# Optimization experiments

Measured on AMD Instinct MI355X. Metric: run time of the kernel, lower is better.

## Reference

```python
import jax, jax.numpy as jnp
import numpy as np
from jax import lax

B, C, H, W = 8, 128, 128, 128


def setup_inputs() -> dict:
    key = jax.random.key(0)
    ks = jax.random.split(key, 10)
    s = 0.02
    return {
        "x": jax.random.normal(ks[0], (B, C, H, W), jnp.float32),
        "ln_w": jnp.ones((C,), jnp.float32),
        "ln_b": jnp.zeros((C,), jnp.float32),
        "qkv_w": jax.random.normal(ks[1], (3 * C, C, 1, 1), jnp.float32) * s,
        "qkv_b": jnp.zeros((3 * C,), jnp.float32),
        "dw_w": jax.random.normal(ks[2], (3 * C, 1, 3, 3), jnp.float32) * s,
        "dw_b": jnp.zeros((3 * C,), jnp.float32),
        "proj_w": jax.random.normal(ks[3], (C, C, 1, 1), jnp.float32) * s,
        "proj_b": jnp.zeros((C,), jnp.float32),
        "temp1": jnp.ones((1, 1), jnp.float32),
        "temp2": jnp.ones((1, 1), jnp.float32),
    }


def reference(x, ln_w, ln_b, qkv_w, qkv_b, dw_w, dw_b, proj_w, proj_b, temp1, temp2):
    Cd = x.shape[1]

    def ln(t):  # WithBias LayerNorm over channel dim (unbiased=False var)
        mu = t.mean(axis=1, keepdims=True)
        var = ((t - mu) ** 2).mean(axis=1, keepdims=True)
        return (t - mu) / jnp.sqrt(var + 1e-5) * ln_w[None, :, None, None] + ln_b[None, :, None, None]

    def conv1(t, w, b):  # 1x1 conv
        return jnp.einsum('bchw,oc->bohw', t, w[:, :, 0, 0]) + b[None, :, None, None]

    def dwc(t):  # depthwise 3x3, pad 1
        y = lax.conv_general_dilated(t, dw_w, (1, 1), ((1, 1), (1, 1)),
                                     dimension_numbers=('NCHW', 'OIHW', 'NCHW'),
                                     feature_group_count=t.shape[1])
        return y + dw_b[None, :, None, None]

    def l2n(t):  # F.normalize over last axis, eps=1e-12
        return t / jnp.maximum(jnp.linalg.norm(t, axis=-1, keepdims=True), 1e-12)

    # ---- stage 1: pool over H, attention over W (channel-pooled) ----
    qkv = dwc(conv1(ln(x), qkv_w, qkv_b))
    q1, k1, v1 = qkv[:, :Cd], qkv[:, Cd:2 * Cd], qkv[:, 2 * Cd:]
    q1 = l2n(q1.mean(axis=2)[:, None])           # [B,1,C,W]
    k1 = l2n(k1.max(axis=2)[:, None])            # [B,1,C,W]
    attn1 = jax.nn.softmax(jnp.einsum('bocw,bocv->bowv', q1, k1) * temp1, axis=-1)  # [B,1,W,W]
    out1 = jnp.einsum('bchw,bowv->bchv', v1, attn1)
    out1 = x + conv1(out1, proj_w, proj_b)

    # ---- stage 2: pool over C, attention over H ----
    qkv = dwc(conv1(ln(out1), qkv_w, qkv_b))
    q2, k2, v2 = qkv[:, :Cd], qkv[:, Cd:2 * Cd], qkv[:, 2 * Cd:]
    q2 = l2n(q2.mean(axis=1)[:, None])           # [B,1,H,W]
    k2 = l2n(k2.mean(axis=1)[:, None])           # [B,1,H,W]
    attn2 = jax.nn.softmax(jnp.einsum('bohw,bogw->bohg', q2, k2) * temp2, axis=-1)  # [B,1,H,H]
    out2 = jnp.einsum('bchw,bohg->bcgw', v2, attn2)  # = (v^T @ attn)^T
    out = conv1(out2, proj_w, proj_b) + out1
    return out
```

## Files before the change

### kernel.cpp

```cpp
#include <hip/hip_runtime.h>

typedef __attribute__((ext_vector_type(8))) short bf16x8;
typedef __attribute__((ext_vector_type(4))) float f32x4;
typedef __attribute__((ext_vector_type(4))) unsigned short us4;
typedef __attribute__((ext_vector_type(4))) unsigned int u32x4;

static constexpr int CC = 128, NN = 16384;
static constexpr int O3 = 384;
static constexpr long long CN  = (long long)CC * NN;
static constexpr long long O3N = (long long)O3 * NN;

__device__ __forceinline__ float wave_sum(float v) {
  for (int o = 32; o; o >>= 1) v += __shfl_xor(v, o);
  return v;
}
__device__ __forceinline__ float wave_max(float v) {
  for (int o = 32; o; o >>= 1) v = fmaxf(v, __shfl_xor(v, o));
  return v;
}
__device__ __forceinline__ unsigned short f2bf(float f) {
  unsigned u = __float_as_uint(f);
  u += 0x7FFF + ((u >> 16) & 1);
  return (unsigned short)(u >> 16);
}
__device__ __forceinline__ float bf2f(unsigned short h) {
  return __uint_as_float((unsigned)h << 16);
}

__global__ __launch_bounds__(64) void k_prep(const float* __restrict__ qkvw,
                                             const float* __restrict__ qkvb,
                                             const float* __restrict__ lnw,
                                             const float* __restrict__ lnb,
                                             const float* __restrict__ projw,
                                             unsigned short* __restrict__ Aq,
                                             unsigned short* __restrict__ Ap,
                                             float* __restrict__ Svec,
                                             float* __restrict__ bias2) {
  int o = blockIdx.x, t = threadIdx.x;
  if (o < O3) {
    float w0 = qkvw[o * 128 + t], w1 = qkvw[o * 128 + t + 64];
    unsigned short h0 = f2bf(w0 * lnw[t]), h1 = f2bf(w1 * lnw[t + 64]);
    Aq[o * 128 + t] = h0; Aq[o * 128 + t + 64] = h1;
    float s = wave_sum(bf2f(h0) + bf2f(h1));
    float bs = wave_sum(w0 * lnb[t] + w1 * lnb[t + 64]);
    if (t == 0) { Svec[o] = s; bias2[o] = qkvb[o] + bs; }
  } else {
    int r = o - O3;
    Ap[r * 128 + t] = f2bf(projw[r * 128 + t]);
    Ap[r * 128 + t + 64] = f2bf(projw[r * 128 + t + 64]);
  }
}

__global__ __launch_bounds__(256) void k_stats(const float* __restrict__ in,
                                               float* __restrict__ mu,
                                               float* __restrict__ rs) {
  int p = blockIdx.x * 256 + threadIdx.x;
  int b = p >> 14, n = p & (NN - 1);
  const float* base = in + (size_t)b * CN + n;
  float s1 = 0.f, s2 = 0.f;
#pragma unroll 8
  for (int c = 0; c < CC; ++c) { float v = base[(size_t)c * NN]; s1 += v; s2 += v * v; }
  float m = s1 * (1.f / CC);
  float var = s2 * (1.f / CC) - m * m;
  mu[p] = m;
  rs[p] = rsqrtf(var + 1e-5f);
}

__global__ __launch_bounds__(256) void k_qkv_mfma(
    const float* __restrict__ x, const float* __restrict__ mu, const float* __restrict__ rs,
    const unsigned short* __restrict__ Aq, const float* __restrict__ Svec,
    const float* __restrict__ bias2, unsigned short* __restrict__ out, int b0) {
  __shared__ unsigned short Bs[64 * 128];
  int bz = blockIdx.z, bg = b0 + bz;
  int n0 = blockIdx.x * 64;
  int t = threadIdx.x, w = t >> 6, l = t & 63;
  int lr = l & 15, lg = l >> 4;
  const float* xb = x + (size_t)bg * CN + n0;

  {
    int n = t & 63, cb = t >> 6;
#pragma unroll
    for (int g = 0; g < 4; ++g) {
      int c8 = (cb * 4 + g) * 8;
      unsigned pk[4];
#pragma unroll
      for (int q = 0; q < 4; ++q) {
        unsigned short a = f2bf(xb[(size_t)(c8 + 2 * q) * NN + n]);
        unsigned short b = f2bf(xb[(size_t)(c8 + 2 * q + 1) * NN + n]);
        pk[q] = (unsigned)a | ((unsigned)b << 16);
      }
      int c8s = c8 ^ ((n & 7) << 3);
      *(u32x4*)&Bs[n * 128 + c8s] = *(const u32x4*)pk;
    }
  }
  __syncthreads();

  f32x4 acc[6][4];
#pragma unroll
  for (int i = 0; i < 6; ++i)
#pragma unroll
    for (int j = 0; j < 4; ++j) acc[i][j] = (f32x4){0.f, 0.f, 0.f, 0.f};

  const unsigned short* Abase = Aq + (size_t)(96 * w + lr) * 128 + lg * 8;
#pragma unroll
  for (int ks = 0; ks < 4; ++ks) {
    bf16x8 bfr[4];
#pragma unroll
    for (int j = 0; j < 4; ++j) {
      int row = 16 * j + lr;
      int col = (ks * 32 + lg * 8) ^ ((lr & 7) << 3);
      bfr[j] = *(const bf16x8*)&Bs[row * 128 + col];
    }
#pragma unroll
    for (int i = 0; i < 6; ++i) {
      bf16x8 afr = *(const bf16x8*)&Abase[(size_t)(16 * i) * 128 + ks * 32];
#pragma unroll
      for (int j = 0; j < 4; ++j)
        acc[i][j] = __builtin_amdgcn_mfma_f32_16x16x32_bf16(afr, bfr[j], acc[i][j], 0, 0, 0);
    }
  }

  float rsv[4], muv[4];
#pragma unroll
  for (int j = 0; j < 4; ++j) {
    int n = n0 + 16 * j + lr;
    rsv[j] = rs[(size_t)bg * NN + n];
    muv[j] = mu[(size_t)bg * NN + n];
  }
#pragma unroll
  for (int i = 0; i < 6; ++i) {
    int ob = 96 * w + 16 * i + lg * 4;
    float sv[4], bv[4];
#pragma unroll
    for (int r2 = 0; r2 < 4; ++r2) { sv[r2] = Svec[ob + r2]; bv[r2] = bias2[ob + r2]; }
#pragma unroll
    for (int j = 0; j < 4; ++j) {
      int n = n0 + 16 * j + lr;
      unsigned short* op = out + (size_t)bz * O3N + n;
#pragma unroll
      for (int r2 = 0; r2 < 4; ++r2)
        op[(size_t)(ob + r2) * NN] = f2bf(rsv[j] * (acc[i][j][r2] - muv[j] * sv[r2]) + bv[r2]);
    }
  }
}

__global__ __launch_bounds__(1024) void k_dwc(unsigned short* __restrict__ buf,
                                              const float* __restrict__ dww,
                                              const float* __restrict__ dwb,
                                              float* __restrict__ qm,
                                              float* __restrict__ km,
                                              int b0, int stage) {
  __shared__ unsigned short pl[130 * 144];
  __shared__ float red[32 * 128];
  int o = blockIdx.x, bz = blockIdx.y, bg = b0 + bz;
  int t = threadIdx.x;
  unsigned short* base = buf + (size_t)bz * O3N + (size_t)o * NN;
  unsigned* pl32 = (unsigned*)pl;

  for (int i = t; i < 1168; i += 1024) {
    int idx;
    if (i < 72) idx = i;
    else if (i < 144) idx = 129 * 72 + (i - 72);
    else { int j = i - 144; int row = (j >> 3) + 1; int s = j & 7;
           idx = row * 72 + (s < 4 ? s : 64 + s); }
    pl32[idx] = 0u;
  }
  __syncthreads();
#pragma unroll
  for (int r = 0; r < 2; ++r) {
    int idx = r * 1024 + t;
    int row = idx >> 4, c8 = (idx & 15) * 8;
    *(u32x4*)&pl[(row + 1) * 144 + 8 + c8] = *(const u32x4*)&base[row * 128 + c8];
  }
  __syncthreads();

  const float* wg = dww + o * 9;
  float w00 = wg[0], w01 = wg[1], w02 = wg[2];
  float w10 = wg[3], w11 = wg[4], w12 = wg[5];
  float w20 = wg[6], w21 = wg[7], w22 = wg[8];
  float bias = dwb[o];
  int mode = (stage == 0) ? (o < 128 ? 1 : (o < 256 ? 2 : 0)) : 0;
  int hh0 = t >> 5, w0 = (t & 31) * 4;
  float csum[4] = {0.f, 0.f, 0.f, 0.f};
  float cmax[4] = {-1e30f, -1e30f, -1e30f, -1e30f};

#pragma unroll
  for (int g = 0; g < 4; ++g) {
    int h = g * 32 + hh0;
    float a0 = bias, a1 = bias, a2 = bias, a3 = bias;
#pragma unroll
    for (int dr = 0; dr < 3; ++dr) {
      const unsigned short* rp = &pl[(h + dr) * 144];
      us4 cA = *(const us4*)&rp[w0 + 4];
      us4 cB = *(const us4*)&rp[w0 + 8];
      us4 cC = *(const us4*)&rp[w0 + 12];
      float f0 = bf2f(cA[3]), f1 = bf2f(cB[0]), f2 = bf2f(cB[1]);
      float f3 = bf2f(cB[2]), f4 = bf2f(cB[3]), f5 = bf2f(cC[0]);
      float wr0 = (dr == 0) ? w00 : (dr == 1 ? w10 : w20);
      float wr1 = (dr == 0) ? w01 : (dr == 1 ? w11 : w21);
      float wr2 = (dr == 0) ? w02 : (dr == 1 ? w12 : w22);
      a0 += f0 * wr0 + f1 * wr1 + f2 * wr2;
      a1 += f1 * wr0 + f2 * wr1 + f3 * wr2;
      a2 += f2 * wr0 + f3 * wr1 + f4 * wr2;
      a3 += f3 * wr0 + f4 * wr1 + f5 * wr2;
    }
    if (mode == 0) {
      us4 ov;
      ov[0] = f2bf(a0); ov[1] = f2bf(a1); ov[2] = f2bf(a2); ov[3] = f2bf(a3);
      *(us4*)&base[g * 4096 + t * 4] = ov;
    } else if (mode == 1) {
      csum[0] += a0; csum[1] += a1; csum[2] += a2; csum[3] += a3;
    } else {
      cmax[0] = fmaxf(cmax[0], a0); cmax[1] = fmaxf(cmax[1], a1);
      cmax[2] = fmaxf(cmax[2], a2); cmax[3] = fmaxf(cmax[3], a3);
    }
  }

  if (mode) {
    int j = t >> 5;
#pragma unroll
    for (int dx = 0; dx < 4; ++dx)
      red[j * 128 + w0 + dx] = (mode == 1) ? csum[dx] : cmax[dx];
    __syncthreads();
    if (t < 128) {
      float v = red[t];
      if (mode == 1) {
        for (int jj = 1; jj < 32; ++jj) v += red[jj * 128 + t];
        qm[(size_t)bg * NN + o * 128 + t] = v * (1.f / 128.f);
      } else {
        for (int jj = 1; jj < 32; ++jj) v = fmaxf(v, red[jj * 128 + t]);
        km[(size_t)bg * NN + (o - 128) * 128 + t] = v;
      }
    }
  }
}

__global__ __launch_bounds__(256) void k_reduce2(const unsigned short* __restrict__ qkv,
                                                 float* __restrict__ qm, float* __restrict__ km,
                                                 int b0) {
  int bz = blockIdx.y;
  int n = blockIdx.x * 256 + threadIdx.x;
  const unsigned short* base = qkv + (size_t)bz * O3N + n;
  float sq = 0.f, sk = 0.f;
#pragma unroll 4
  for (int c = 0; c < 128; ++c) {
    sq += bf2f(base[(size_t)c * NN]);
    sk += bf2f(base[(size_t)(c + 128) * NN]);
  }
  size_t off = (size_t)(b0 + bz) * NN + n;
  qm[off] = sq * (1.f / 128.f);
  km[off] = sk * (1.f / 128.f);
}

__global__ void k_norm2(float* __restrict__ qm, float* __restrict__ km, int row0) {
  float* buf = blockIdx.y ? km : qm;
  int r = row0 + blockIdx.x, t = threadIdx.x;
  float* p = buf + (size_t)r * 128;
  float v0 = p[t], v1 = p[t + 64];
  float s = wave_sum(v0 * v0 + v1 * v1);
  float sc = 1.f / fmaxf(sqrtf(s), 1e-12f);
  p[t] = v0 * sc;
  p[t + 64] = v1 * sc;
}

__global__ void k_attn1(const float* __restrict__ qm, const float* __restrict__ km,
                        const float* __restrict__ temp, unsigned short* __restrict__ attnT,
                        int b0) {
  int bg = b0 + blockIdx.y;
  int i = blockIdx.x, t = threadIdx.x;
  const float* qb = qm + (size_t)bg * NN;
  const float* kb = km + (size_t)bg * NN;
  __shared__ float qcol[128];
  __shared__ float wred[2];
  qcol[t] = qb[t * 128 + i];
  __syncthreads();
  float s = 0.f;
#pragma unroll 4
  for (int k = 0; k < 128; ++k) s += qcol[k] * kb[k * 128 + t];
  s *= temp[0];
  int wid = t >> 6, lane = t & 63;
  float mx = wave_max(s);
  if (lane == 0) wred[wid] = mx;
  __syncthreads();
  mx = fmaxf(wred[0], wred[1]);
  float pv = __expf(s - mx);
  __syncthreads();
  float sm = wave_sum(pv);
  if (lane == 0) wred[wid] = sm;
  __syncthreads();
  float denom = wred[0] + wred[1];
  attnT[(size_t)bg * NN + (size_t)t * 128 + i] = f2bf(pv / denom);
}

__global__ void k_attn2(const float* __restrict__ qm, const float* __restrict__ km,
                        const float* __restrict__ temp, unsigned short* __restrict__ attnT,
                        int b0) {
  int bg = b0 + blockIdx.y;
  int i = blockIdx.x, t = threadIdx.x;
  const float* qb = qm + (size_t)bg * NN + i * 128;
  const float* kb = km + (size_t)bg * NN + (size_t)t * 128;
  __shared__ float qrow[128];
  __shared__ float wred[2];
  qrow[t] = qb[t];
  __syncthreads();
  float s = 0.f;
#pragma unroll 4
  for (int w = 0; w < 128; ++w) s += qrow[w] * kb[w];
  s *= temp[0];
  int wid = t >> 6, lane = t & 63;
  float mx = wave_max(s);
  if (lane == 0) wred[wid] = mx;
  __syncthreads();
  mx = fmaxf(wred[0], wred[1]);
  float pv = __expf(s - mx);
  __syncthreads();
  float sm = wave_sum(pv);
  if (lane == 0) wred[wid] = sm;
  __syncthreads();
  float denom = wred[0] + wred[1];
  attnT[(size_t)bg * NN + (size_t)t * 128 + i] = f2bf(pv / denom);
}

__global__ __launch_bounds__(256) void k_apply1_mfma(unsigned short* __restrict__ buf,
                                                     const unsigned short* __restrict__ attnT,
                                                     int b0) {
  __shared__ unsigned short Al[128 * 136];
  __shared__ unsigned short Bl[128 * 136];
  int bz = blockIdx.z, bg = b0 + bz;
  int m0 = blockIdx.x * 128;
  int t = threadIdx.x, w = t >> 6, l = t & 63, lr = l & 15, lg = l >> 4;
  const unsigned short* asrc = buf + (size_t)bz * O3N + (size_t)256 * NN + (size_t)m0 * 128;
  const unsigned short* bsrc = attnT + (size_t)bg * NN;
#pragma unroll
  for (int r = 0; r < 8; ++r) {
    int idx = r * 256 + t;
    int row = idx >> 4, c8 = (idx & 15) * 8;
    *(u32x4*)&Al[row * 136 + c8] = *(const u32x4*)&asrc[row * 128 + c8];
    *(u32x4*)&Bl[row * 136 + c8] = *(const u32x4*)&bsrc[row * 128 + c8];
  }
  __syncthreads();
  f32x4 acc[2][8];
#pragma unroll
  for (int i = 0; i < 2; ++i)
#pragma unroll
    for (int j = 0; j < 8; ++j) acc[i][j] = (f32x4){0.f, 0.f, 0.f, 0.f};
#pragma unroll
  for (int ks = 0; ks < 4; ++ks) {
    bf16x8 bfr[8];
#pragma unroll
    for (int j = 0; j < 8; ++j)
      bfr[j] = *(const bf16x8*)&Bl[(16 * j + lr) * 136 + ks * 32 + lg * 8];
#pragma unroll
    for (int i = 0; i < 2; ++i) {
      bf16x8 afr = *(const bf16x8*)&Al[(32 * w + 16 * i + lr) * 136 + ks * 32 + lg * 8];
#pragma unroll
      for (int j = 0; j < 8; ++j)
        acc[i][j] = __builtin_amdgcn_mfma_f32_16x16x32_bf16(afr, bfr[j], acc[i][j], 0, 0, 0);
    }
  }
  unsigned short* ob = buf + (size_t)bz * O3N;
#pragma unroll
  for (int i = 0; i < 2; ++i)
#pragma unroll
    for (int j = 0; j < 8; ++j)
#pragma unroll
      for (int r2 = 0; r2 < 4; ++r2) {
        int m = m0 + 32 * w + 16 * i + lg * 4 + r2;
        int n = 16 * j + lr;
        ob[(size_t)m * 128 + n] = f2bf(acc[i][j][r2]);
      }
}

__global__ __launch_bounds__(256) void k_apply2_mfma(unsigned short* __restrict__ buf,
                                                     const unsigned short* __restrict__ attnT,
                                                     int b0) {
  __shared__ unsigned short At[128 * 136];
  __shared__ unsigned short Bt[128 * 136];
  int bz = blockIdx.z, bg = b0 + bz, c = blockIdx.x;
  int t = threadIdx.x, w = t >> 6, l = t & 63, lr = l & 15, lg = l >> 4;
  const unsigned short* vsrc = buf + (size_t)bz * O3N + (size_t)(256 + c) * NN;
  const unsigned short* asrc = attnT + (size_t)bg * NN;
#pragma unroll
  for (int r = 0; r < 8; ++r) {
    int idx = r * 256 + t;
    int row = idx >> 4, c8 = (idx & 15) * 8;
    *(u32x4*)&At[row * 136 + c8] = *(const u32x4*)&asrc[row * 128 + c8];
    us4 lo = *(const us4*)&vsrc[row * 128 + c8];
    us4 hi = *(const us4*)&vsrc[row * 128 + c8 + 4];
#pragma unroll
    for (int q = 0; q < 4; ++q) {
      Bt[(c8 + q) * 136 + row] = lo[q];
      Bt[(c8 + 4 + q) * 136 + row] = hi[q];
    }
  }
  __syncthreads();
  f32x4 acc[2][8];
#pragma unroll
  for (int i = 0; i < 2; ++i)
#pragma unroll
    for (int j = 0; j < 8; ++j) acc[i][j] = (f32x4){0.f, 0.f, 0.f, 0.f};
#pragma unroll
  for (int ks = 0; ks < 4; ++ks) {
    bf16x8 bfr[8];
#pragma unroll
    for (int j = 0; j < 8; ++j)
      bfr[j] = *(const bf16x8*)&Bt[(16 * j + lr) * 136 + ks * 32 + lg * 8];
#pragma unroll
    for (int i = 0; i < 2; ++i) {
      bf16x8 afr = *(const bf16x8*)&At[(32 * w + 16 * i + lr) * 136 + ks * 32 + lg * 8];
#pragma unroll
      for (int j = 0; j < 8; ++j)
        acc[i][j] = __builtin_amdgcn_mfma_f32_16x16x32_bf16(afr, bfr[j], acc[i][j], 0, 0, 0);
    }
  }
  unsigned short* ob = buf + (size_t)bz * O3N + (size_t)c * NN;
#pragma unroll
  for (int i = 0; i < 2; ++i)
#pragma unroll
    for (int j = 0; j < 8; ++j)
#pragma unroll
      for (int r2 = 0; r2 < 4; ++r2) {
        int g = 32 * w + 16 * i + lg * 4 + r2;
        int n = 16 * j + lr;
        ob[(size_t)g * 128 + n] = f2bf(acc[i][j][r2]);
      }
}

__global__ __launch_bounds__(256) void k_proj_mfma(
    const unsigned short* __restrict__ tin, const unsigned short* __restrict__ Ap,
    const float* __restrict__ pb, const float* __restrict__ res,
    float* __restrict__ dst, float* __restrict__ mu, float* __restrict__ rs,
    int b0, int do_stats) {
  __shared__ unsigned short Bs2[64 * 128];
  __shared__ float red1[64 * 17];
  __shared__ float red2[64 * 17];
  int bz = blockIdx.z, bg = b0 + bz;
  int n0 = blockIdx.x * 64;
  int t = threadIdx.x, w = t >> 6, l = t & 63, lr = l & 15, lg = l >> 4;
  const unsigned short* tb = tin + (size_t)bz * O3N + n0;

  {
    int n = t & 63, cb = t >> 6;
#pragma unroll
    for (int g = 0; g < 4; ++g) {
      int c8 = (cb * 4 + g) * 8;
      unsigned pk[4];
#pragma unroll
      for (int q = 0; q < 4; ++q) {
        unsigned short a = tb[(size_t)(c8 + 2 * q) * NN + n];
        unsigned short b = tb[(size_t)(c8 + 2 * q + 1) * NN + n];
        pk[q] = (unsigned)a | ((unsigned)b << 16);
      }
      int c8s = c8 ^ ((n & 7) << 3);
      *(u32x4*)&Bs2[n * 128 + c8s] = *(const u32x4*)pk;
    }
  }
  __syncthreads();

  f32x4 acc[2][4];
#pragma unroll
  for (int i = 0; i < 2; ++i)
#pragma unroll
    for (int j = 0; j < 4; ++j) acc[i][j] = (f32x4){0.f, 0.f, 0.f, 0.f};

  const unsigned short* Abase = Ap + (size_t)(32 * w + lr) * 128 + lg * 8;
#pragma unroll
  for (int ks = 0; ks < 4; ++ks) {
    bf16x8 bfr[4];
#pragma unroll
    for (int j = 0; j < 4; ++j) {
      int row = 16 * j + lr;
      int col = (ks * 32 + lg * 8) ^ ((lr & 7) << 3);
      bfr[j] = *(const bf16x8*)&Bs2[row * 128 + col];
    }
#pragma unroll
    for (int i = 0; i < 2; ++i) {
      bf16x8 afr = *(const bf16x8*)&Abase[(size_t)(16 * i) * 128 + ks * 32];
#pragma unroll
      for (int j = 0; j < 4; ++j)
        acc[i][j] = __builtin_amdgcn_mfma_f32_16x16x32_bf16(afr, bfr[j], acc[i][j], 0, 0, 0);
    }
  }

  float s1p[4] = {0.f, 0.f, 0.f, 0.f}, s2p[4] = {0.f, 0.f, 0.f, 0.f};
#pragma unroll
  for (int i = 0; i < 2; ++i) {
    int ob = 32 * w + 16 * i + lg * 4;
    float bv[4];
#pragma unroll
    for (int r2 = 0; r2 < 4; ++r2) bv[r2] = pb[ob + r2];
#pragma unroll
    for (int j = 0; j < 4; ++j) {
      int n = n0 + 16 * j + lr;
#pragma unroll
      for (int r2 = 0; r2 < 4; ++r2) {
        size_t off = (size_t)bg * CN + (size_t)(ob + r2) * NN + n;
        float val = acc[i][j][r2] + bv[r2] + res[off];
        dst[off] = val;
        s1p[j] += val;
        s2p[j] += val * val;
      }
    }
  }
  if (do_stats) {
#pragma unroll
    for (int j = 0; j < 4; ++j) {
      red1[(16 * j + lr) * 17 + (w * 4 + lg)] = s1p[j];
      red2[(16 * j + lr) * 17 + (w * 4 + lg)] = s2p[j];
    }
    __syncthreads();
    if (t < 64) {
      float s1 = 0.f, s2 = 0.f;
#pragma unroll
      for (int kk = 0; kk < 16; ++kk) { s1 += red1[t * 17 + kk]; s2 += red2[t * 17 + kk]; }
      float m = s1 * (1.f / 128.f);
      float var = s2 * (1.f / 128.f) - m * m;
      mu[(size_t)bg * NN + n0 + t] = m;
      rs[(size_t)bg * NN + n0 + t] = rsqrtf(var + 1e-5f);
    }
  }
}

extern "C" void kernel_launch(void* const* d_in, const int* in_sizes, int n_in,
                              void* d_out, int out_size, void* d_ws, size_t ws_size,
                              hipStream_t stream) {
  (void)in_sizes; (void)n_in; (void)out_size;
  const float* x     = (const float*)d_in[0];
  const float* lnw   = (const float*)d_in[1];
  const float* lnb   = (const float*)d_in[2];
  const float* qkvw  = (const float*)d_in[3];
  const float* qkvb  = (const float*)d_in[4];
  const float* dww   = (const float*)d_in[5];
  const float* dwb   = (const float*)d_in[6];
  const float* projw = (const float*)d_in[7];
  const float* projb = (const float*)d_in[8];
  const float* temp1 = (const float*)d_in[9];
  const float* temp2 = (const float*)d_in[10];
  float* out = (float*)d_out;
  float* ws = (float*)d_ws;

  auto needBytes = [&](int nb) {
    return ((size_t)nb * (O3N / 2) + 4ull * 131072 + 65536 + 768 + 24576 + 8192) * 4;
  };
  int NB = 8;
  while (NB > 1 && ws_size < needBytes(NB)) NB >>= 1;
  if (ws_size < needBytes(1)) return;

  unsigned short* convbuf = (unsigned short*)ws;
  float* mu = ws + (size_t)NB * (O3N / 2);
  float* rs = mu + 131072;
  float* qm = rs + 131072;
  float* km = qm + 131072;
  unsigned short* attnT = (unsigned short*)(km + 131072);
  float* Svec  = (float*)(attnT + 8ull * NN);
  float* bias2 = Svec + 384;
  unsigned short* Aq = (unsigned short*)(bias2 + 384);
  unsigned short* Ap = Aq + 49152;

  k_prep<<<512, 64, 0, stream>>>(qkvw, qkvb, lnw, lnb, projw, Aq, Ap, Svec, bias2);
  k_stats<<<512, 256, 0, stream>>>(x, mu, rs);

  for (int stage = 0; stage < 2; ++stage) {
    const float* src = stage ? out : x;
    for (int b0 = 0; b0 < 8; b0 += NB) {
      k_qkv_mfma<<<dim3(256, 1, NB), 256, 0, stream>>>(src, mu, rs, Aq, Svec, bias2, convbuf, b0);
      k_dwc<<<dim3(384, NB), 1024, 0, stream>>>(convbuf, dww, dwb, qm, km, b0, stage);
      if (stage == 1)
        k_reduce2<<<dim3(64, NB), 256, 0, stream>>>(convbuf, qm, km, b0);
      k_norm2<<<dim3(NB * 128, 2), 64, 0, stream>>>(qm, km, b0 * 128);
      if (stage == 0)
        k_attn1<<<dim3(128, NB), 128, 0, stream>>>(qm, km, temp1, attnT, b0);
      else
        k_attn2<<<dim3(128, NB), 128, 0, stream>>>(qm, km, temp2, attnT, b0);
      if (stage == 0)
        k_apply1_mfma<<<dim3(128, 1, NB), 256, 0, stream>>>(convbuf, attnT, b0);
      else
        k_apply2_mfma<<<dim3(128, 1, NB), 256, 0, stream>>>(convbuf, attnT, b0);
      const float* resp = stage ? out : x;
      k_proj_mfma<<<dim3(256, 1, NB), 256, 0, stream>>>(convbuf, Ap, projb, resp, out,
                                                        mu, rs, b0, stage == 0 ? 1 : 0);
    }
  }
}
```

Before: 338.8 us.

## Fuse stage-1 LayerNorm stats into QKV kernel and preload weight fragments

```diff
diff --git a/kernel.cpp b/kernel.cpp
--- a/kernel.cpp
+++ b/kernel.cpp
@@ -51,42 +51,44 @@
   }
 }
 
-__global__ __launch_bounds__(256) void k_stats(const float* __restrict__ in,
-                                               float* __restrict__ mu,
-                                               float* __restrict__ rs) {
-  int p = blockIdx.x * 256 + threadIdx.x;
-  int b = p >> 14, n = p & (NN - 1);
-  const float* base = in + (size_t)b * CN + n;
-  float s1 = 0.f, s2 = 0.f;
-#pragma unroll 8
-  for (int c = 0; c < CC; ++c) { float v = base[(size_t)c * NN]; s1 += v; s2 += v * v; }
-  float m = s1 * (1.f / CC);
-  float var = s2 * (1.f / CC) - m * m;
-  mu[p] = m;
-  rs[p] = rsqrtf(var + 1e-5f);
-}
-
-__global__ __launch_bounds__(256) void k_qkv_mfma(
+__global__ __launch_bounds__(256, 2) void k_qkv_mfma(
     const float* __restrict__ x, const float* __restrict__ mu, const float* __restrict__ rs,
     const unsigned short* __restrict__ Aq, const float* __restrict__ Svec,
-    const float* __restrict__ bias2, unsigned short* __restrict__ out, int b0) {
+    const float* __restrict__ bias2, unsigned short* __restrict__ out, int b0, int useg) {
   __shared__ unsigned short Bs[64 * 128];
+  __shared__ float muL[64], rsL[64];
   int bz = blockIdx.z, bg = b0 + bz;
   int n0 = blockIdx.x * 64;
   int t = threadIdx.x, w = t >> 6, l = t & 63;
   int lr = l & 15, lg = l >> 4;
   const float* xb = x + (size_t)bg * CN + n0;
 
+  bf16x8 afr[6][4];
+  {
+    const unsigned short* Abase = Aq + (size_t)(96 * w + lr) * 128 + lg * 8;
+#pragma unroll
+    for (int i = 0; i < 6; ++i)
+#pragma unroll
+      for (int ks = 0; ks < 4; ++ks)
+        afr[i][ks] = *(const bf16x8*)&Abase[(size_t)(16 * i) * 128 + ks * 32];
+  }
+
   {
     int n = t & 63, cb = t >> 6;
+    float xr[32];
+#pragma unroll
+    for (int g = 0; g < 4; ++g)
+#pragma unroll
+      for (int q = 0; q < 8; ++q)
+        xr[g * 8 + q] = xb[(size_t)((cb * 4 + g) * 8 + q) * NN + n];
 #pragma unroll
     for (int g = 0; g < 4; ++g) {
       int c8 = (cb * 4 + g) * 8;
       unsigned pk[4];
 #pragma unroll
       for (int q = 0; q < 4; ++q) {
-        unsigned short a = f2bf(xb[(size_t)(c8 + 2 * q) * NN + n]);
-        unsigned short b = f2bf(xb[(size_t)(c8 + 2 * q + 1) * NN + n]);
+        unsigned short a = f2bf(xr[g * 8 + 2 * q]);
+        unsigned short b = f2bf(xr[g * 8 + 2 * q + 1]);
         pk[q] = (unsigned)a | ((unsigned)b << 16);
       }
       int c8s = c8 ^ ((n & 7) << 3);
@@ -95,13 +97,35 @@
   }
   __syncthreads();
 
+  if (!useg) {
+    int p = t >> 2, sub = t & 3;
+    float s1 = 0.f, s2 = 0.f;
+#pragma unroll
+    for (int b2 = 0; b2 < 4; ++b2) {
+      int c8 = (sub * 4 + b2) * 8;
+      int c8s = c8 ^ ((p & 7) << 3);
+      bf16x8 v = *(const bf16x8*)&Bs[p * 128 + c8s];
+#pragma unroll
+      for (int q = 0; q < 8; ++q) {
+        float f = bf2f((unsigned short)v[q]);
+        s1 += f; s2 += f * f;
+      }
+    }
+    s1 += __shfl_xor(s1, 1); s2 += __shfl_xor(s2, 1);
+    s1 += __shfl_xor(s1, 2); s2 += __shfl_xor(s2, 2);
+    if (sub == 0) {
+      float m = s1 * (1.f / 128.f);
+      muL[p] = m;
+      rsL[p] = rsqrtf(s2 * (1.f / 128.f) - m * m + 1e-5f);
+    }
+  }
+  __syncthreads();
+
   f32x4 acc[6][4];
 #pragma unroll
   for (int i = 0; i < 6; ++i)
 #pragma unroll
     for (int j = 0; j < 4; ++j) acc[i][j] = (f32x4){0.f, 0.f, 0.f, 0.f};
-
-  const unsigned short* Abase = Aq + (size_t)(96 * w + lr) * 128 + lg * 8;
 #pragma unroll
   for (int ks = 0; ks < 4; ++ks) {
     bf16x8 bfr[4];
@@ -112,20 +136,23 @@
       bfr[j] = *(const bf16x8*)&Bs[row * 128 + col];
     }
 #pragma unroll
-    for (int i = 0; i < 6; ++i) {
-      bf16x8 afr = *(const bf16x8*)&Abase[(size_t)(16 * i) * 128 + ks * 32];
+    for (int i = 0; i < 6; ++i)
 #pragma unroll
       for (int j = 0; j < 4; ++j)
-        acc[i][j] = __builtin_amdgcn_mfma_f32_16x16x32_bf16(afr, bfr[j], acc[i][j], 0, 0, 0);
-    }
+        acc[i][j] = __builtin_amdgcn_mfma_f32_16x16x32_bf16(afr[i][ks], bfr[j], acc[i][j], 0, 0, 0);
   }
 
   float rsv[4], muv[4];
 #pragma unroll
   for (int j = 0; j < 4; ++j) {
-    int n = n0 + 16 * j + lr;
-    rsv[j] = rs[(size_t)bg * NN + n];
-    muv[j] = mu[(size_t)bg * NN + n];
+    int nl = 16 * j + lr;
+    if (useg) {
+      rsv[j] = rs[(size_t)bg * NN + n0 + nl];
+      muv[j] = mu[(size_t)bg * NN + n0 + nl];
+    } else {
+      rsv[j] = rsL[nl];
+      muv[j] = muL[nl];
+    }
   }
 #pragma unroll
   for (int i = 0; i < 6; ++i) {
@@ -439,18 +466,31 @@
   int t = threadIdx.x, w = t >> 6, l = t & 63, lr = l & 15, lg = l >> 4;
   const unsigned short* tb = tin + (size_t)bz * O3N + n0;
 
+  bf16x8 afr[2][4];
+  {
+    const unsigned short* Abase = Ap + (size_t)(32 * w + lr) * 128 + lg * 8;
+#pragma unroll
+    for (int i = 0; i < 2; ++i)
+#pragma unroll
+      for (int ks = 0; ks < 4; ++ks)
+        afr[i][ks] = *(const bf16x8*)&Abase[(size_t)(16 * i) * 128 + ks * 32];
+  }
+
   {
     int n = t & 63, cb = t >> 6;
+    unsigned short vr[32];
+#pragma unroll
+    for (int g = 0; g < 4; ++g)
+#pragma unroll
+      for (int q = 0; q < 8; ++q)
+        vr[g * 8 + q] = tb[(size_t)((cb * 4 + g) * 8 + q) * NN + n];
 #pragma unroll
     for (int g = 0; g < 4; ++g) {
       int c8 = (cb * 4 + g) * 8;
       unsigned pk[4];
 #pragma unroll
-      for (int q = 0; q < 4; ++q) {
-        unsigned short a = tb[(size_t)(c8 + 2 * q) * NN + n];
-        unsigned short b = tb[(size_t)(c8 + 2 * q + 1) * NN + n];
-        pk[q] = (unsigned)a | ((unsigned)b << 16);
-      }
+      for (int q = 0; q < 4; ++q)
+        pk[q] = (unsigned)vr[g * 8 + 2 * q] | ((unsigned)vr[g * 8 + 2 * q + 1] << 16);
       int c8s = c8 ^ ((n & 7) << 3);
       *(u32x4*)&Bs2[n * 128 + c8s] = *(const u32x4*)pk;
     }
@@ -463,7 +503,6 @@
 #pragma unroll
     for (int j = 0; j < 4; ++j) acc[i][j] = (f32x4){0.f, 0.f, 0.f, 0.f};
 
-  const unsigned short* Abase = Ap + (size_t)(32 * w + lr) * 128 + lg * 8;
 #pragma unroll
   for (int ks = 0; ks < 4; ++ks) {
     bf16x8 bfr[4];
@@ -474,12 +513,10 @@
       bfr[j] = *(const bf16x8*)&Bs2[row * 128 + col];
     }
 #pragma unroll
-    for (int i = 0; i < 2; ++i) {
-      bf16x8 afr = *(const bf16x8*)&Abase[(size_t)(16 * i) * 128 + ks * 32];
+    for (int i = 0; i < 2; ++i)
 #pragma unroll
       for (int j = 0; j < 4; ++j)
-        acc[i][j] = __builtin_amdgcn_mfma_f32_16x16x32_bf16(afr, bfr[j], acc[i][j], 0, 0, 0);
-    }
+        acc[i][j] = __builtin_amdgcn_mfma_f32_16x16x32_bf16(afr[i][ks], bfr[j], acc[i][j], 0, 0, 0);
   }
 
   float s1p[4] = {0.f, 0.f, 0.f, 0.f}, s2p[4] = {0.f, 0.f, 0.f, 0.f};
@@ -558,12 +595,12 @@
   unsigned short* Ap = Aq + 49152;
 
   k_prep<<<512, 64, 0, stream>>>(qkvw, qkvb, lnw, lnb, projw, Aq, Ap, Svec, bias2);
-  k_stats<<<512, 256, 0, stream>>>(x, mu, rs);
 
   for (int stage = 0; stage < 2; ++stage) {
     const float* src = stage ? out : x;
     for (int b0 = 0; b0 < 8; b0 += NB) {
-      k_qkv_mfma<<<dim3(256, 1, NB), 256, 0, stream>>>(src, mu, rs, Aq, Svec, bias2, convbuf, b0);
+      k_qkv_mfma<<<dim3(256, 1, NB), 256, 0, stream>>>(src, mu, rs, Aq, Svec, bias2, convbuf,
+                                                       b0, stage);
       k_dwc<<<dim3(384, NB), 1024, 0, stream>>>(convbuf, dww, dwb, qm, km, b0, stage);
       if (stage == 1)
         k_reduce2<<<dim3(64, NB), 256, 0, stream>>>(convbuf, qm, km, b0);
```

Result: faster. 311.7 us (-8.0%).
